# Performance work log

Hardware: AMD Instinct MI355X
Metric: run time of the kernel (lower is better)

The kernel has to match this reference:

```python
import jax, jax.numpy as jnp
import numpy as np

D_IN = 1024
D_OUT = 1024
N, S = 4, 2048

def setup_inputs() -> dict:
    key = jax.random.key(0)
    kv, kk, kq, k1, k2, k3 = jax.random.split(key, 6)
    return {
        "v": jax.random.normal(kv, (N, S, D_IN), dtype=jnp.float32),
        "k": jax.random.normal(kk, (N, S, D_IN), dtype=jnp.float32),
        "q": jax.random.normal(kq, (N, S, D_IN), dtype=jnp.float32),
        "WV": jax.random.normal(k1, (D_OUT, D_IN), dtype=jnp.float32),
        "WQ": jax.random.normal(k2, (D_OUT, D_IN), dtype=jnp.float32),
        "WK": jax.random.normal(k3, (D_OUT, D_IN), dtype=jnp.float32),
    }

def reference(v, k, q, WV, WQ, WK) -> jnp.ndarray:
    # projections: x @ W.T  -> [N, S, D_OUT]
    wv = jnp.einsum('nsw,ow->nso', v, WV)
    wk = jnp.einsum('nsw,ow->nso', k, WK)
    wq = jnp.einsum('nsw,ow->nso', q, WQ)
    # scores [N, Sq, Sk]; NOTE: softmax over axis=1 (query axis, matching torch dim=1),
    # then post-hoc division by input_shape[0] AFTER softmax (faithful to source).
    scores = jnp.einsum('nqo,nko->nqk', wq, wk)
    wqk = jax.nn.softmax(scores, axis=1) / jnp.float32(D_IN)
    return jnp.einsum('nqk,nko->nqo', wqk, wv)
```

## Files before the change

### kernel.cpp

```cpp
#include <hip/hip_runtime.h>
#include <math.h>


typedef _Float16 f16;
typedef _Float16 f16x8 __attribute__((ext_vector_type(8)));
typedef float f32x4 __attribute__((ext_vector_type(4)));

enum StageMode { SM_F32SPLIT, SM_F32HI, SM_PLANES2, SM_PLANES1, SM_EXP };
enum EpiMode   { EPI_F32, EPI_SPLIT, EPI_F16T };

#define LDS_PITCH 40

template<StageMode SM>
__device__ __forceinline__ void stage_tile(const void* __restrict__ P0,
                                           const void* __restrict__ P1,
                                           const float* __restrict__ pM,
                                           const float* __restrict__ pR,
                                           f16* __restrict__ Shi, f16* __restrict__ Slo,
                                           long rowBase, int ld, int k0, int tid)
{
    if constexpr (SM == SM_PLANES2 || SM == SM_PLANES1) {
        const f16* gh = (const f16*)P0;
        const f16* gl = (const f16*)P1;
#pragma unroll
        for (int i = 0; i < 2; i++) {
            int c  = tid + i * 256;
            int r  = c >> 2;
            int cc = c & 3;
            long g = (rowBase + r) * (long)ld + k0 + cc * 8;
            *(uint4*)&Shi[r * LDS_PITCH + cc * 8] = *(const uint4*)&gh[g];
            if constexpr (SM == SM_PLANES2)
                *(uint4*)&Slo[r * LDS_PITCH + cc * 8] = *(const uint4*)&gl[g];
        }
    } else {
        const float* gf = (const float*)P0;
#pragma unroll
        for (int i = 0; i < 2; i++) {
            int c  = tid + i * 256;
            int r  = c >> 2;
            int cc = c & 3;
            long g = (rowBase + r) * (long)ld + k0 + cc * 8;
            float4 x0 = *(const float4*)&gf[g];
            float4 x1 = *(const float4*)&gf[g + 4];
            float xs[8] = {x0.x, x0.y, x0.z, x0.w, x1.x, x1.y, x1.z, x1.w};
            if constexpr (SM == SM_EXP) {
                float4 ma = *(const float4*)&pM[k0 + cc * 8];
                float4 mb = *(const float4*)&pM[k0 + cc * 8 + 4];
                float4 ra = *(const float4*)&pR[k0 + cc * 8];
                float4 rb = *(const float4*)&pR[k0 + cc * 8 + 4];
                float ms[8] = {ma.x, ma.y, ma.z, ma.w, mb.x, mb.y, mb.z, mb.w};
                float rs[8] = {ra.x, ra.y, ra.z, ra.w, rb.x, rb.y, rb.z, rb.w};
                f16x8 h;
#pragma unroll
                for (int e = 0; e < 8; e++)
                    h[e] = (f16)(__expf(xs[e] - ms[e]) * rs[e]);
                *(f16x8*)&Shi[r * LDS_PITCH + cc * 8] = h;
            } else if constexpr (SM == SM_F32HI) {
                f16x8 h;
#pragma unroll
                for (int e = 0; e < 8; e++) h[e] = (f16)xs[e];
                *(f16x8*)&Shi[r * LDS_PITCH + cc * 8] = h;
            } else {
                f16x8 h, l;
#pragma unroll
                for (int e = 0; e < 8; e++) {
                    f16 hh = (f16)xs[e];
                    h[e] = hh;
                    l[e] = (f16)(xs[e] - (float)hh);
                }
                *(f16x8*)&Shi[r * LDS_PITCH + cc * 8] = h;
                *(f16x8*)&Slo[r * LDS_PITCH + cc * 8] = l;
            }
        }
    }
}

template<StageMode SA, StageMode SB, EpiMode EP>
__global__ __launch_bounds__(256, 2)
void mfma_gemm(const void* __restrict__ Ahi, const void* __restrict__ Alo,
               const void* __restrict__ Bhi, const void* __restrict__ Blo,
               const float* __restrict__ statM, const float* __restrict__ statR,
               void* __restrict__ C0, void* __restrict__ C1,
               int M, int Nc, int K, int lda, int ldb, int ldc,
               long batchA, long batchB, long batchC,
               float epiScale, int tsShift)
{
    constexpr bool TRIPLE = (SA == SM_F32SPLIT || SA == SM_PLANES2);

    int bx, by;
    {
        const int GM = 4;
        int gx = gridDim.x;
        int lin = blockIdx.y * gx + blockIdx.x;
        int nig = GM * gx;
        int gid = lin / nig;
        int rem = lin - gid * nig;
        by = gid * GM + (rem % GM);
        bx = rem / GM;
    }
    const int n0 = bx * 128;
    const int m0 = by * 128;
    const long z = blockIdx.z;

    long aOfs = z * batchA, bOfs = z * batchB, cOfs = z * batchC;
    const float* pM = statM + z * (long)K;
    const float* pR = statR + z * (long)K;

    __shared__ __align__(16) f16 As_hi[128 * LDS_PITCH];
    __shared__ __align__(16) f16 Bs_hi[128 * LDS_PITCH];
    __shared__ __align__(16) f16 As_lo[TRIPLE ? 128 * LDS_PITCH : 8];
    __shared__ __align__(16) f16 Bs_lo[TRIPLE ? 128 * LDS_PITCH : 8];

    const int tid  = threadIdx.x;
    const int lane = tid & 63;
    const int wave = tid >> 6;
    const int wr = (wave >> 1) * 64;
    const int wc = (wave & 1) * 64;
    const int fm = lane & 15;
    const int fk = (lane >> 4) * 8;

    f32x4 acc[4][4];
#pragma unroll
    for (int i = 0; i < 4; i++)
#pragma unroll
        for (int j = 0; j < 4; j++) acc[i][j] = (f32x4){0.f, 0.f, 0.f, 0.f};

    for (int k0 = 0; k0 < K; k0 += 32) {
        {
            const void* a0 = (SA == SM_F32SPLIT || SA == SM_F32HI || SA == SM_EXP)
                           ? (const void*)((const float*)Ahi + aOfs)
                           : (const void*)((const f16*)Ahi + aOfs);
            const void* a1 = (SA == SM_PLANES2) ? (const void*)((const f16*)Alo + aOfs) : nullptr;
            stage_tile<SA>(a0, a1, pM, pR, As_hi, As_lo, m0, lda, k0, tid);
        }
        {
            const void* b0 = (SB == SM_F32SPLIT || SB == SM_F32HI)
                           ? (const void*)((const float*)Bhi + bOfs)
                           : (const void*)((const f16*)Bhi + bOfs);
            const void* b1 = (SB == SM_PLANES2) ? (const void*)((const f16*)Blo + bOfs) : nullptr;
            stage_tile<SB>(b0, b1, nullptr, nullptr, Bs_hi, Bs_lo, n0, ldb, k0, tid);
        }
        __syncthreads();

        f16x8 ah[4], bh[4], al[4], bl[4];
#pragma unroll
        for (int i = 0; i < 4; i++) {
            int ro = (wr + i * 16 + fm) * LDS_PITCH + fk;
            int co = (wc + i * 16 + fm) * LDS_PITCH + fk;
            ah[i] = *(const f16x8*)&As_hi[ro];
            bh[i] = *(const f16x8*)&Bs_hi[co];
            if constexpr (TRIPLE) {
                al[i] = *(const f16x8*)&As_lo[ro];
                bl[i] = *(const f16x8*)&Bs_lo[co];
            }
        }
#pragma unroll
        for (int i = 0; i < 4; i++) {
#pragma unroll
            for (int j = 0; j < 4; j++) {
                acc[i][j] = __builtin_amdgcn_mfma_f32_16x16x32_f16(ah[i], bh[j], acc[i][j], 0, 0, 0);
                if constexpr (TRIPLE) {
                    acc[i][j] = __builtin_amdgcn_mfma_f32_16x16x32_f16(ah[i], bl[j], acc[i][j], 0, 0, 0);
                    acc[i][j] = __builtin_amdgcn_mfma_f32_16x16x32_f16(al[i], bh[j], acc[i][j], 0, 0, 0);
                }
            }
        }
        __syncthreads();
    }

    const int cr = (lane >> 4) * 4;
    const int cn = lane & 15;
#pragma unroll
    for (int i = 0; i < 4; i++) {
#pragma unroll
        for (int j = 0; j < 4; j++) {
#pragma unroll
            for (int r = 0; r < 4; r++) {
                long mg = m0 + wr + i * 16 + cr + r;
                long ng = n0 + wc + j * 16 + cn;
                float val = acc[i][j][r] * epiScale;
                if constexpr (EP == EPI_F32) {
                    ((float*)C0)[cOfs + mg * ldc + ng] = val;
                } else if constexpr (EP == EPI_SPLIT) {
                    f16 h = (f16)val;
                    ((f16*)C0)[cOfs + mg * ldc + ng] = h;
                    ((f16*)C1)[cOfs + mg * ldc + ng] = (f16)(val - (float)h);
                } else {
                    long TS = 1L << tsShift;
                    long nb = mg >> tsShift;
                    long s  = mg & (TS - 1);
                    long addr = nb * ((long)Nc << tsShift) + ng * TS + s;
                    ((f16*)C0)[addr] = (f16)val;
                }
            }
        }
    }
}

__global__ __launch_bounds__(256)
void stats_partial_kernel(const float* __restrict__ Sc,
                          float* __restrict__ pm, float* __restrict__ ps, int S)
{
    const int n = blockIdx.z, qc = blockIdx.y;
    const int c = threadIdx.x & 63, qs = threadIdx.x >> 6;
    const int kk = blockIdx.x * 64 + c;
    const float* Sn = Sc + (long)n * S * S;
    float m = -INFINITY, s = 0.f;
    const int q0 = qc * 128;
    for (int q = q0 + qs; q < q0 + 128; q += 4) {
        float x = Sn[(long)q * S + kk];
        float nm = fmaxf(m, x);
        s = s * __expf(m - nm) + __expf(x - nm);
        m = nm;
    }
    __shared__ float rm[4][64], rs[4][64];
    rm[qs][c] = m; rs[qs][c] = s;
    __syncthreads();
    if (qs == 0) {
        float M = fmaxf(fmaxf(rm[0][c], rm[1][c]), fmaxf(rm[2][c], rm[3][c]));
        float Ssum = rs[0][c] * __expf(rm[0][c] - M) + rs[1][c] * __expf(rm[1][c] - M)
                   + rs[2][c] * __expf(rm[2][c] - M) + rs[3][c] * __expf(rm[3][c] - M);
        long o = ((long)n * 16 + qc) * S + kk;
        pm[o] = M; ps[o] = Ssum;
    }
}

__global__ __launch_bounds__(64)
void stats_combine_kernel(const float* __restrict__ pm, const float* __restrict__ ps,
                          float* __restrict__ statM, float* __restrict__ statR, int S)
{
    const int n = blockIdx.y;
    const int kk = blockIdx.x * 64 + threadIdx.x;
    float M = -INFINITY;
#pragma unroll
    for (int i = 0; i < 16; i++)
        M = fmaxf(M, pm[((long)n * 16 + i) * S + kk]);
    float Ssum = 0.f;
#pragma unroll
    for (int i = 0; i < 16; i++)
        Ssum += ps[((long)n * 16 + i) * S + kk] * __expf(pm[((long)n * 16 + i) * S + kk] - M);
    statM[(long)n * S + kk] = M;
    statR[(long)n * S + kk] = 1.0f / Ssum;
}

extern "C" void kernel_launch(void* const* d_in, const int* in_sizes, int n_in,
                              void* d_out, int out_size, void* d_ws, size_t ws_size,
                              hipStream_t stream)
{
    const float* v  = (const float*)d_in[0];
    const float* k  = (const float*)d_in[1];
    const float* q  = (const float*)d_in[2];
    const float* WV = (const float*)d_in[3];
    const float* WQ = (const float*)d_in[4];
    const float* WK = (const float*)d_in[5];
    float* out = (float*)d_out;

    const int N = 4, S = 2048, D = 1024;
    const long NSD = (long)N * S * D;
    const long NSS = (long)N * S * S;

    f16* ws = (f16*)d_ws;
    f16* wq_hi = ws;
    f16* wq_lo = ws + NSD;
    f16* wk_hi = ws + 2 * NSD;
    f16* wk_lo = ws + 3 * NSD;
    f16* wvT_hi = ws + 4 * NSD;
    float* Sc   = (float*)(ws + 5 * NSD);
    float* pm    = (float*)(ws + 9 * NSD);
    float* ps    = pm + (long)N * 16 * S;
    float* statM = ps + (long)N * 16 * S;
    float* statR = statM + (long)N * S;

    dim3 blk(256);

    {
        dim3 g(D / 128, (N * S) / 128, 1);
        mfma_gemm<SM_F32SPLIT, SM_F32SPLIT, EPI_SPLIT><<<g, blk, 0, stream>>>(
            q, nullptr, WQ, nullptr, nullptr, nullptr, wq_hi, wq_lo,
            N * S, D, D, D, D, D, 0, 0, 0, 1.0f, 0);
        mfma_gemm<SM_F32SPLIT, SM_F32SPLIT, EPI_SPLIT><<<g, blk, 0, stream>>>(
            k, nullptr, WK, nullptr, nullptr, nullptr, wk_hi, wk_lo,
            N * S, D, D, D, D, D, 0, 0, 0, 1.0f, 0);
        mfma_gemm<SM_F32HI, SM_F32HI, EPI_F16T><<<g, blk, 0, stream>>>(
            v, nullptr, WV, nullptr, nullptr, nullptr, wvT_hi, nullptr,
            N * S, D, D, D, D, 0, 0, 0, 0, 1.0f, 11 );
    }
    {
        dim3 g(S / 128, S / 128, N);
        mfma_gemm<SM_PLANES2, SM_PLANES2, EPI_F32><<<g, blk, 0, stream>>>(
            wq_hi, wq_lo, wk_hi, wk_lo, nullptr, nullptr, Sc, nullptr,
            S, S, D, D, D, S, (long)S * D, (long)S * D, (long)S * S, 1.0f, 0);
    }
    {
        dim3 gA(S / 64, S / 128, N);
        stats_partial_kernel<<<gA, blk, 0, stream>>>(Sc, pm, ps, S);
        dim3 gB(S / 64, N);
        stats_combine_kernel<<<gB, dim3(64), 0, stream>>>(pm, ps, statM, statR, S);
    }
    {
        dim3 g(D / 128, S / 128, N);
        mfma_gemm<SM_EXP, SM_PLANES1, EPI_F32><<<g, blk, 0, stream>>>(
            Sc, nullptr, wvT_hi, nullptr, statM, statR, out, nullptr,
            S, D, S, S, S, D, (long)S * S, (long)S * D, (long)S * D, 1.0f / (float)D, 0);
    }
}
```

Baseline: 493.8 us.

## Fuse column softmax stats into score GEMM, stage f16 planes via global_load_lds

Computes the per-column partial max and sum-exp in the score GEMM's epilogue, which removes the separate stats_partial pass that re-read the full fp32 score matrix. Half-precision operand planes are now staged with global_load_lds straight into an XOR-swizzled, unpadded LDS layout instead of going through registers. Launch bounds are raised to 4 blocks per SM. The final GEMM also drops the grouped tile swizzle. The extra epilogue reduction adds shuffles and exps, and the tighter register budget may cause spills in the triple-MFMA kernels.

```diff
diff --git a/kernel.cpp b/kernel.cpp
--- a/kernel.cpp
+++ b/kernel.cpp
@@ -9,94 +9,114 @@
 enum StageMode { SM_F32SPLIT, SM_F32HI, SM_PLANES2, SM_PLANES1, SM_EXP };
 enum EpiMode   { EPI_F32, EPI_SPLIT, EPI_F16T };
 
-#define LDS_PITCH 40
+#define PAD_PITCH 40
+#define GLL_PITCH 32
+
+__device__ __forceinline__ void gll16(const f16* g, f16* l) {
+    __builtin_amdgcn_global_load_lds(
+        (const __attribute__((address_space(1))) void*)g,
+        (__attribute__((address_space(3))) void*)l, 16, 0, 0);
+}
+
+__device__ __forceinline__ void stage_gll_plane(const f16* __restrict__ gplane,
+                                                f16* __restrict__ lds,
+                                                long rowBase, int ld, int k0,
+                                                int wave, int lane)
+{
+#pragma unroll
+    for (int i = 0; i < 2; i++) {
+        int slotBase = (wave * 2 + i) * 64;
+        int t = slotBase + lane;
+        int r = t >> 2;
+        int c = (t & 3) ^ ((r >> 1) & 3);
+        const f16* g = gplane + (rowBase + r) * (long)ld + k0 + c * 8;
+        gll16(g, lds + (long)slotBase * 8);
+    }
+}
+
+__device__ __forceinline__ int frag_off_gll(int row, int g) {
+    return row * GLL_PITCH + ((g ^ ((row >> 1) & 3)) << 3);
+}
+__device__ __forceinline__ int frag_off_pad(int row, int g) {
+    return row * PAD_PITCH + (g << 3);
+}
 
 template<StageMode SM>
-__device__ __forceinline__ void stage_tile(const void* __restrict__ P0,
-                                           const void* __restrict__ P1,
-                                           const float* __restrict__ pM,
-                                           const float* __restrict__ pR,
-                                           f16* __restrict__ Shi, f16* __restrict__ Slo,
-                                           long rowBase, int ld, int k0, int tid)
-{
-    if constexpr (SM == SM_PLANES2 || SM == SM_PLANES1) {
-        const f16* gh = (const f16*)P0;
-        const f16* gl = (const f16*)P1;
-#pragma unroll
-        for (int i = 0; i < 2; i++) {
-            int c  = tid + i * 256;
-            int r  = c >> 2;
-            int cc = c & 3;
-            long g = (rowBase + r) * (long)ld + k0 + cc * 8;
-            *(uint4*)&Shi[r * LDS_PITCH + cc * 8] = *(const uint4*)&gh[g];
-            if constexpr (SM == SM_PLANES2)
-                *(uint4*)&Slo[r * LDS_PITCH + cc * 8] = *(const uint4*)&gl[g];
-        }
-    } else {
-        const float* gf = (const float*)P0;
-#pragma unroll
-        for (int i = 0; i < 2; i++) {
-            int c  = tid + i * 256;
-            int r  = c >> 2;
-            int cc = c & 3;
-            long g = (rowBase + r) * (long)ld + k0 + cc * 8;
-            float4 x0 = *(const float4*)&gf[g];
-            float4 x1 = *(const float4*)&gf[g + 4];
-            float xs[8] = {x0.x, x0.y, x0.z, x0.w, x1.x, x1.y, x1.z, x1.w};
-            if constexpr (SM == SM_EXP) {
-                float4 ma = *(const float4*)&pM[k0 + cc * 8];
-                float4 mb = *(const float4*)&pM[k0 + cc * 8 + 4];
-                float4 ra = *(const float4*)&pR[k0 + cc * 8];
-                float4 rb = *(const float4*)&pR[k0 + cc * 8 + 4];
-                float ms[8] = {ma.x, ma.y, ma.z, ma.w, mb.x, mb.y, mb.z, mb.w};
-                float rs[8] = {ra.x, ra.y, ra.z, ra.w, rb.x, rb.y, rb.z, rb.w};
-                f16x8 h;
-#pragma unroll
-                for (int e = 0; e < 8; e++)
-                    h[e] = (f16)(__expf(xs[e] - ms[e]) * rs[e]);
-                *(f16x8*)&Shi[r * LDS_PITCH + cc * 8] = h;
-            } else if constexpr (SM == SM_F32HI) {
-                f16x8 h;
-#pragma unroll
-                for (int e = 0; e < 8; e++) h[e] = (f16)xs[e];
-                *(f16x8*)&Shi[r * LDS_PITCH + cc * 8] = h;
-            } else {
-                f16x8 h, l;
-#pragma unroll
-                for (int e = 0; e < 8; e++) {
-                    f16 hh = (f16)xs[e];
-                    h[e] = hh;
-                    l[e] = (f16)(xs[e] - (float)hh);
-                }
-                *(f16x8*)&Shi[r * LDS_PITCH + cc * 8] = h;
-                *(f16x8*)&Slo[r * LDS_PITCH + cc * 8] = l;
-            }
-        }
-    }
-}
-
-template<StageMode SA, StageMode SB, EpiMode EP>
-__global__ __launch_bounds__(256, 2)
+__device__ __forceinline__ void stage_f32_tile(const float* __restrict__ gf,
+                                               const float* __restrict__ pM,
+                                               const float* __restrict__ pR,
+                                               f16* __restrict__ Shi, f16* __restrict__ Slo,
+                                               long rowBase, int ld, int k0, int tid)
+{
+#pragma unroll
+    for (int i = 0; i < 2; i++) {
+        int c  = tid + i * 256;
+        int r  = c >> 2;
+        int cc = c & 3;
+        long g = (rowBase + r) * (long)ld + k0 + cc * 8;
+        float4 x0 = *(const float4*)&gf[g];
+        float4 x1 = *(const float4*)&gf[g + 4];
+        float xs[8] = {x0.x, x0.y, x0.z, x0.w, x1.x, x1.y, x1.z, x1.w};
+        if constexpr (SM == SM_EXP) {
+            float4 ma = *(const float4*)&pM[k0 + cc * 8];
+            float4 mb = *(const float4*)&pM[k0 + cc * 8 + 4];
+            float4 ra = *(const float4*)&pR[k0 + cc * 8];
+            float4 rb = *(const float4*)&pR[k0 + cc * 8 + 4];
+            float ms[8] = {ma.x, ma.y, ma.z, ma.w, mb.x, mb.y, mb.z, mb.w};
+            float rs[8] = {ra.x, ra.y, ra.z, ra.w, rb.x, rb.y, rb.z, rb.w};
+            f16x8 h;
+#pragma unroll
+            for (int e = 0; e < 8; e++)
+                h[e] = (f16)(__expf(xs[e] - ms[e]) * rs[e]);
+            *(f16x8*)&Shi[r * PAD_PITCH + cc * 8] = h;
+        } else if constexpr (SM == SM_F32HI) {
+            f16x8 h;
+#pragma unroll
+            for (int e = 0; e < 8; e++) h[e] = (f16)xs[e];
+            *(f16x8*)&Shi[r * PAD_PITCH + cc * 8] = h;
+        } else {
+            f16x8 h, l;
+#pragma unroll
+            for (int e = 0; e < 8; e++) {
+                f16 hh = (f16)xs[e];
+                h[e] = hh;
+                l[e] = (f16)(xs[e] - (float)hh);
+            }
+            *(f16x8*)&Shi[r * PAD_PITCH + cc * 8] = h;
+            *(f16x8*)&Slo[r * PAD_PITCH + cc * 8] = l;
+        }
+    }
+}
+
+template<StageMode SA, StageMode SB, EpiMode EP, int GROUPM, bool STATS>
+__global__ __launch_bounds__(256, 4)
 void mfma_gemm(const void* __restrict__ Ahi, const void* __restrict__ Alo,
                const void* __restrict__ Bhi, const void* __restrict__ Blo,
                const float* __restrict__ statM, const float* __restrict__ statR,
+               float* __restrict__ pmOut, float* __restrict__ psOut,
                void* __restrict__ C0, void* __restrict__ C1,
                int M, int Nc, int K, int lda, int ldb, int ldc,
                long batchA, long batchB, long batchC,
                float epiScale, int tsShift)
 {
     constexpr bool TRIPLE = (SA == SM_F32SPLIT || SA == SM_PLANES2);
+    constexpr bool A_GLL  = (SA == SM_PLANES2 || SA == SM_PLANES1);
+    constexpr bool B_GLL  = (SB == SM_PLANES2 || SB == SM_PLANES1);
+    constexpr int A_SZ = A_GLL ? 128 * GLL_PITCH : 128 * PAD_PITCH;
+    constexpr int B_SZ = B_GLL ? 128 * GLL_PITCH : 128 * PAD_PITCH;
 
     int bx, by;
-    {
-        const int GM = 4;
+    if constexpr (GROUPM > 0) {
         int gx = gridDim.x;
         int lin = blockIdx.y * gx + blockIdx.x;
-        int nig = GM * gx;
+        int nig = GROUPM * gx;
         int gid = lin / nig;
         int rem = lin - gid * nig;
-        by = gid * GM + (rem % GM);
-        bx = rem / GM;
+        by = gid * GROUPM + (rem % GROUPM);
+        bx = rem / GROUPM;
+    } else {
+        bx = blockIdx.x;
+        by = blockIdx.y;
     }
     const int n0 = bx * 128;
     const int m0 = by * 128;
@@ -106,10 +126,10 @@
     const float* pM = statM + z * (long)K;
     const float* pR = statR + z * (long)K;
 
-    __shared__ __align__(16) f16 As_hi[128 * LDS_PITCH];
-    __shared__ __align__(16) f16 Bs_hi[128 * LDS_PITCH];
-    __shared__ __align__(16) f16 As_lo[TRIPLE ? 128 * LDS_PITCH : 8];
-    __shared__ __align__(16) f16 Bs_lo[TRIPLE ? 128 * LDS_PITCH : 8];
+    __shared__ __align__(16) f16 As_hi[A_SZ];
+    __shared__ __align__(16) f16 Bs_hi[B_SZ];
+    __shared__ __align__(16) f16 As_lo[TRIPLE ? A_SZ : 8];
+    __shared__ __align__(16) f16 Bs_lo[TRIPLE ? B_SZ : 8];
 
     const int tid  = threadIdx.x;
     const int lane = tid & 63;
@@ -117,7 +137,8 @@
     const int wr = (wave >> 1) * 64;
     const int wc = (wave & 1) * 64;
     const int fm = lane & 15;
-    const int fk = (lane >> 4) * 8;
+    const int fg = lane >> 4;
+    const int fk = fg * 8;
 
     f32x4 acc[4][4];
 #pragma unroll
@@ -125,33 +146,42 @@
 #pragma unroll
         for (int j = 0; j < 4; j++) acc[i][j] = (f32x4){0.f, 0.f, 0.f, 0.f};
 
+    int roA[4], roB[4];
+#pragma unroll
+    for (int i = 0; i < 4; i++) {
+        int rowA = wr + i * 16 + fm;
+        int rowB = wc + i * 16 + fm;
+        roA[i] = A_GLL ? frag_off_gll(rowA, fg) : frag_off_pad(rowA, fg);
+        roB[i] = B_GLL ? frag_off_gll(rowB, fg) : frag_off_pad(rowB, fg);
+    }
+
     for (int k0 = 0; k0 < K; k0 += 32) {
-        {
-            const void* a0 = (SA == SM_F32SPLIT || SA == SM_F32HI || SA == SM_EXP)
-                           ? (const void*)((const float*)Ahi + aOfs)
-                           : (const void*)((const f16*)Ahi + aOfs);
-            const void* a1 = (SA == SM_PLANES2) ? (const void*)((const f16*)Alo + aOfs) : nullptr;
-            stage_tile<SA>(a0, a1, pM, pR, As_hi, As_lo, m0, lda, k0, tid);
-        }
-        {
-            const void* b0 = (SB == SM_F32SPLIT || SB == SM_F32HI)
-                           ? (const void*)((const float*)Bhi + bOfs)
-                           : (const void*)((const f16*)Bhi + bOfs);
-            const void* b1 = (SB == SM_PLANES2) ? (const void*)((const f16*)Blo + bOfs) : nullptr;
-            stage_tile<SB>(b0, b1, nullptr, nullptr, Bs_hi, Bs_lo, n0, ldb, k0, tid);
+        if constexpr (SA == SM_PLANES2) {
+            stage_gll_plane((const f16*)Ahi + aOfs, As_hi, m0, lda, k0, wave, lane);
+            stage_gll_plane((const f16*)Alo + aOfs, As_lo, m0, lda, k0, wave, lane);
+        } else if constexpr (SA == SM_PLANES1) {
+            stage_gll_plane((const f16*)Ahi + aOfs, As_hi, m0, lda, k0, wave, lane);
+        } else {
+            stage_f32_tile<SA>((const float*)Ahi + aOfs, pM, pR, As_hi, As_lo, m0, lda, k0, tid);
+        }
+        if constexpr (SB == SM_PLANES2) {
+            stage_gll_plane((const f16*)Bhi + bOfs, Bs_hi, n0, ldb, k0, wave, lane);
+            stage_gll_plane((const f16*)Blo + bOfs, Bs_lo, n0, ldb, k0, wave, lane);
+        } else if constexpr (SB == SM_PLANES1) {
+            stage_gll_plane((const f16*)Bhi + bOfs, Bs_hi, n0, ldb, k0, wave, lane);
+        } else {
+            stage_f32_tile<SB>((const float*)Bhi + bOfs, nullptr, nullptr, Bs_hi, Bs_lo, n0, ldb, k0, tid);
         }
         __syncthreads();
 
         f16x8 ah[4], bh[4], al[4], bl[4];
 #pragma unroll
         for (int i = 0; i < 4; i++) {
-            int ro = (wr + i * 16 + fm) * LDS_PITCH + fk;
-            int co = (wc + i * 16 + fm) * LDS_PITCH + fk;
-            ah[i] = *(const f16x8*)&As_hi[ro];
-            bh[i] = *(const f16x8*)&Bs_hi[co];
+            ah[i] = *(const f16x8*)&As_hi[roA[i]];
+            bh[i] = *(const f16x8*)&Bs_hi[roB[i]];
             if constexpr (TRIPLE) {
-                al[i] = *(const f16x8*)&As_lo[ro];
-                bl[i] = *(const f16x8*)&Bs_lo[co];
+                al[i] = *(const f16x8*)&As_lo[roA[i]];
+                bl[i] = *(const f16x8*)&Bs_lo[roB[i]];
             }
         }
 #pragma unroll
@@ -168,8 +198,8 @@
         __syncthreads();
     }
 
-    const int cr = (lane >> 4) * 4;
-    const int cn = lane & 15;
+    const int cr = fg * 4;
+    const int cn = fm;
 #pragma unroll
     for (int i = 0; i < 4; i++) {
 #pragma unroll
@@ -195,33 +225,44 @@
             }
         }
     }
-}
-
-__global__ __launch_bounds__(256)
-void stats_partial_kernel(const float* __restrict__ Sc,
-                          float* __restrict__ pm, float* __restrict__ ps, int S)
-{
-    const int n = blockIdx.z, qc = blockIdx.y;
-    const int c = threadIdx.x & 63, qs = threadIdx.x >> 6;
-    const int kk = blockIdx.x * 64 + c;
-    const float* Sn = Sc + (long)n * S * S;
-    float m = -INFINITY, s = 0.f;
-    const int q0 = qc * 128;
-    for (int q = q0 + qs; q < q0 + 128; q += 4) {
-        float x = Sn[(long)q * S + kk];
-        float nm = fmaxf(m, x);
-        s = s * __expf(m - nm) + __expf(x - nm);
-        m = nm;
-    }
-    __shared__ float rm[4][64], rs[4][64];
-    rm[qs][c] = m; rs[qs][c] = s;
-    __syncthreads();
-    if (qs == 0) {
-        float M = fmaxf(fmaxf(rm[0][c], rm[1][c]), fmaxf(rm[2][c], rm[3][c]));
-        float Ssum = rs[0][c] * __expf(rm[0][c] - M) + rs[1][c] * __expf(rm[1][c] - M)
-                   + rs[2][c] * __expf(rm[2][c] - M) + rs[3][c] * __expf(rm[3][c] - M);
-        long o = ((long)n * 16 + qc) * S + kk;
-        pm[o] = M; ps[o] = Ssum;
+
+    if constexpr (STATS) {
+        __shared__ float stM[2][128];
+        __shared__ float stS[2][128];
+#pragma unroll
+        for (int j = 0; j < 4; j++) {
+            float mj = -3.402823466e38f;
+#pragma unroll
+            for (int i = 0; i < 4; i++)
+#pragma unroll
+                for (int r = 0; r < 4; r++) mj = fmaxf(mj, acc[i][j][r]);
+            float sj = 0.f;
+#pragma unroll
+            for (int i = 0; i < 4; i++)
+#pragma unroll
+                for (int r = 0; r < 4; r++) sj += __expf(acc[i][j][r] - mj);
+#pragma unroll
+            for (int mask = 16; mask <= 32; mask <<= 1) {
+                float mo = __shfl_xor(mj, mask, 64);
+                float so = __shfl_xor(sj, mask, 64);
+                float mn = fmaxf(mj, mo);
+                sj = sj * __expf(mj - mn) + so * __expf(mo - mn);
+                mj = mn;
+            }
+            if (fg == 0) {
+                stM[wave >> 1][wc + j * 16 + cn] = mj;
+                stS[wave >> 1][wc + j * 16 + cn] = sj;
+            }
+        }
+        __syncthreads();
+        if (tid < 128) {
+            float ma = stM[0][tid], mb = stM[1][tid];
+            float Mc = fmaxf(ma, mb);
+            float Sv = stS[0][tid] * __expf(ma - Mc) + stS[1][tid] * __expf(mb - Mc);
+            long o = ((long)z * (M >> 7) + by) * (long)Nc + (long)bx * 128 + tid;
+            pmOut[o] = Mc;
+            psOut[o] = Sv;
+        }
     }
 }
 
@@ -275,32 +316,30 @@
 
     {
         dim3 g(D / 128, (N * S) / 128, 1);
-        mfma_gemm<SM_F32SPLIT, SM_F32SPLIT, EPI_SPLIT><<<g, blk, 0, stream>>>(
-            q, nullptr, WQ, nullptr, nullptr, nullptr, wq_hi, wq_lo,
+        mfma_gemm<SM_F32SPLIT, SM_F32SPLIT, EPI_SPLIT, 4, false><<<g, blk, 0, stream>>>(
+            q, nullptr, WQ, nullptr, nullptr, nullptr, nullptr, nullptr, wq_hi, wq_lo,
             N * S, D, D, D, D, D, 0, 0, 0, 1.0f, 0);
-        mfma_gemm<SM_F32SPLIT, SM_F32SPLIT, EPI_SPLIT><<<g, blk, 0, stream>>>(
-            k, nullptr, WK, nullptr, nullptr, nullptr, wk_hi, wk_lo,
+        mfma_gemm<SM_F32SPLIT, SM_F32SPLIT, EPI_SPLIT, 4, false><<<g, blk, 0, stream>>>(
+            k, nullptr, WK, nullptr, nullptr, nullptr, nullptr, nullptr, wk_hi, wk_lo,
             N * S, D, D, D, D, D, 0, 0, 0, 1.0f, 0);
-        mfma_gemm<SM_F32HI, SM_F32HI, EPI_F16T><<<g, blk, 0, stream>>>(
-            v, nullptr, WV, nullptr, nullptr, nullptr, wvT_hi, nullptr,
+        mfma_gemm<SM_F32HI, SM_F32HI, EPI_F16T, 4, false><<<g, blk, 0, stream>>>(
+            v, nullptr, WV, nullptr, nullptr, nullptr, nullptr, nullptr, wvT_hi, nullptr,
             N * S, D, D, D, D, 0, 0, 0, 0, 1.0f, 11 );
     }
     {
         dim3 g(S / 128, S / 128, N);
-        mfma_gemm<SM_PLANES2, SM_PLANES2, EPI_F32><<<g, blk, 0, stream>>>(
-            wq_hi, wq_lo, wk_hi, wk_lo, nullptr, nullptr, Sc, nullptr,
+        mfma_gemm<SM_PLANES2, SM_PLANES2, EPI_F32, 4, true><<<g, blk, 0, stream>>>(
+            wq_hi, wq_lo, wk_hi, wk_lo, nullptr, nullptr, pm, ps, Sc, nullptr,
             S, S, D, D, D, S, (long)S * D, (long)S * D, (long)S * S, 1.0f, 0);
     }
     {
-        dim3 gA(S / 64, S / 128, N);
-        stats_partial_kernel<<<gA, blk, 0, stream>>>(Sc, pm, ps, S);
         dim3 gB(S / 64, N);
         stats_combine_kernel<<<gB, dim3(64), 0, stream>>>(pm, ps, statM, statR, S);
     }
     {
         dim3 g(D / 128, S / 128, N);
-        mfma_gemm<SM_EXP, SM_PLANES1, EPI_F32><<<g, blk, 0, stream>>>(
-            Sc, nullptr, wvT_hi, nullptr, statM, statR, out, nullptr,
+        mfma_gemm<SM_EXP, SM_PLANES1, EPI_F32, 0, false><<<g, blk, 0, stream>>>(
+            Sc, nullptr, wvT_hi, nullptr, statM, statR, nullptr, nullptr, out, nullptr,
             S, D, S, S, S, D, (long)S * S, (long)S * D, (long)S * D, 1.0f / (float)D, 0);
     }
 }
```

After: 531.2 us. 7.6% more time.
